# Optimization experiments

Hardware: AMD Instinct MI355X
Metric: run time of the kernel (lower is better)

Reference implementation:

```python
import jax, jax.numpy as jnp
import numpy as np

RADIUS = 0.4
NSAMPLE = 32


def setup_inputs() -> dict:
    key = jax.random.key(0)
    ks = jax.random.split(key, 6)
    B, N, C = 2, 16384, 64
    xyz = jax.random.normal(ks[0], (B, N, 3), jnp.float32)
    features = jax.random.normal(ks[1], (B, C, N), jnp.float32)

    def w(k, i, o):
        return jax.random.normal(k, (i, o), jnp.float32) * (1.0 / np.sqrt(i))

    W1 = w(ks[2], C + 3, 64)
    W2 = w(ks[3], 64, 64)
    W3 = w(ks[4], 64, 128)
    return {
        "xyz": xyz, "features": features,
        "W1": W1, "b1": jnp.zeros((64,), jnp.float32),
        "W2": W2, "b2": jnp.zeros((64,), jnp.float32),
        "W3": W3, "b3": jnp.zeros((128,), jnp.float32),
        "npoint": 4096,
    }


def ball_query(xyz, new_xyz, radius, nsample):
    """xyz [B,N,3], new_xyz [B,S,3] -> neighbor idx [B,S,nsample] int32.
    Replicates pointnet2 ball_query: first `nsample` points (in index order)
    within `radius` of each centroid; empty slots filled with the first hit
    (0 if no point is in range)."""
    N = xyz.shape[1]
    # squared distances [B,S,N] via ||a||^2 + ||b||^2 - 2 a.b
    d2 = (jnp.sum(new_xyz * new_xyz, -1)[:, :, None]
          + jnp.sum(xyz * xyz, -1)[:, None, :]
          - 2.0 * jnp.einsum('bsc,bnc->bsn', new_xyz, xyz))
    cand = jnp.where(d2 < radius * radius,
                     jnp.arange(N, dtype=jnp.int32), jnp.int32(N))
    neg_topk, _ = jax.lax.top_k(-cand, nsample)  # nsample smallest indices
    idx = -neg_topk
    first = idx[..., :1]
    idx = jnp.where(idx == N, first, idx)  # pad with first valid neighbor
    idx = jnp.where(idx == N, 0, idx)      # no neighbor at all -> 0
    return idx


def reference(xyz, features, W1, b1, W2, b2, W3, b3, npoint):
    B = xyz.shape[0]
    # sample_method=None, keep_first_half=False -> idx = arange(npoint)
    new_xyz = xyz[:, :npoint]                        # [B,S,3]
    idx = ball_query(jax.lax.stop_gradient(xyz),
                     jax.lax.stop_gradient(new_xyz), RADIUS, NSAMPLE)
    # group: gather neighbors, re-center xyz, concat features (use_xyz=True)
    grouped_xyz = jax.vmap(lambda p, i: p[i])(xyz, idx) - new_xyz[:, :, None]  # [B,S,K,3]
    feats_nc = features.transpose(0, 2, 1)           # [B,N,C]
    grouped_f = jax.vmap(lambda f, i: f[i])(feats_nc, idx)  # [B,S,K,C]
    g = jnp.concatenate([grouped_xyz, grouped_f], axis=-1)  # [B,S,K,3+C]
    # shared MLP (1x1 convs + ReLU)
    h = jax.nn.relu(jnp.einsum('bskc,cd->bskd', g, W1) + b1)
    h = jax.nn.relu(jnp.einsum('bskc,cd->bskd', h, W2) + b2)
    h = jax.nn.relu(jnp.einsum('bskc,cd->bskd', h, W3) + b3)
    new_features = jnp.max(h, axis=2).transpose(0, 2, 1)    # [B,128,S]
    samp_idx = jnp.tile(jnp.arange(npoint, dtype=jnp.int32), (B, 1))
    return new_xyz, new_features, samp_idx
```

## Files before the change

kernel.cpp:

```cpp
#include <hip/hip_runtime.h>

#define BB 2
#define NN 16384
#define CC 64
#define SS 4096
#define KK 32
#define R2 0.16f

#define GD   24
#define GC   (GD * GD * GD)
#define GCP  (GC + 4)
#define CAP  512
#define CAPL (CAP / 64)

typedef __bf16 bf16x8 __attribute__((ext_vector_type(8)));
typedef float  f32x4  __attribute__((ext_vector_type(4)));

#define MFMA(a, b, c) __builtin_amdgcn_mfma_f32_16x16x32_bf16((a), (b), (c), 0, 0, 0)

static __device__ __forceinline__ ushort f2bf(float f) {
    __bf16 h = (__bf16)f;
    return *(ushort*)&h;
}

static __device__ __forceinline__ int cellc(float x) {
    int i = (int)floorf(x * 2.5f + 12.0f);
    return i < 0 ? 0 : (i > GD - 1 ? GD - 1 : i);
}

#define WS_PTS4   0
#define WS_FEAT   524288
#define WS_W1T    4718592
#define WS_W2T    4730880
#define WS_W3T    4739072
#define WS_SPTS   4755456
#define WS_SSID   5279744
#define WS_CELLS  5410816
#define WS_OFF    5476352

#define T_PTS   (BB * NN)
#define T_W1    (T_PTS + 64 * 96)
#define T_W2    (T_W1 + 64 * 64)
#define T_W3    (T_W2 + 128 * 64)
#define T_NXYZ  (T_W3 + BB * SS * 3)
#define T_SIDX  (T_NXYZ + BB * SS)
#define T_ALL   (T_SIDX + BB * NN * 8)

__global__ __launch_bounds__(256) void prep_kernel(
        const float* __restrict__ xyz, const float* __restrict__ feat,
        const float* __restrict__ W1, const float* __restrict__ W2,
        const float* __restrict__ W3,
        float4* __restrict__ pts4, ushort* __restrict__ feat_nc,
        ushort* __restrict__ W1t, ushort* __restrict__ W2t,
        ushort* __restrict__ W3t,
        float* __restrict__ out_xyz, float* __restrict__ out_sidx,
        ushort* __restrict__ cells) {
    const int t = blockIdx.x * 256 + threadIdx.x;
    if (t < T_PTS) {
        const float* p = xyz + (size_t)t * 3;
        const float x = p[0], y = p[1], z = p[2];
        pts4[t] = make_float4(x, y, z, x * x + y * y + z * z);
        cells[t] = (ushort)((cellc(z) * GD + cellc(y)) * GD + cellc(x));
    } else if (t < T_W1) {
        const int i = t - T_PTS;
        const int n = i / 96, k = i - n * 96;
        float v = 0.0f;
        if (k < 64) v = W1[(3 + k) * 64 + n];
        else if (k < 67) v = W1[(k - 64) * 64 + n];
        W1t[n * 96 + k] = f2bf(v);
    } else if (t < T_W2) {
        const int i = t - T_W1;
        const int n = i >> 6, k = i & 63;
        W2t[n * 64 + k] = f2bf(W2[k * 64 + n]);
    } else if (t < T_W3) {
        const int i = t - T_W2;
        const int n = i >> 6, k = i & 63;
        W3t[n * 64 + k] = f2bf(W3[k * 128 + n]);
    } else if (t < T_NXYZ) {
        const int i = t - T_W3;
        const int b = i / (SS * 3), j = i - b * (SS * 3);
        out_xyz[i] = xyz[(size_t)b * NN * 3 + j];
    } else if (t < T_SIDX) {
        const int i = t - T_NXYZ;
        out_sidx[i] = (float)(i & (SS - 1));
    } else if (t < T_ALL) {
        const int j = t - T_SIDX;
        const int nl = j >> 3, c8 = j & 7;
        const int b = nl >> 14, n = nl & (NN - 1);
        const float* fb = feat + (size_t)b * CC * NN + n;
        uint u[4];
        #pragma unroll
        for (int q = 0; q < 4; ++q) {
            const float f0 = fb[(size_t)(c8 * 8 + 2 * q) * NN];
            const float f1 = fb[(size_t)(c8 * 8 + 2 * q + 1) * NN];
            u[q] = (uint)f2bf(f0) | ((uint)f2bf(f1) << 16);
        }
        *(uint4*)(feat_nc + (size_t)nl * 64 + c8 * 8) = make_uint4(u[0], u[1], u[2], u[3]);
    }
}

#define CH 14
__global__ __launch_bounds__(1024) void bin_kernel(
        const float4* __restrict__ pts4, const ushort* __restrict__ cells,
        float4* __restrict__ spts, int* __restrict__ ssid,
        uint* __restrict__ offs) {
    __shared__ uint hist[GC];
    __shared__ uint wsum[17];
    const int b = blockIdx.x, t = threadIdx.x;
    const ushort* cb = cells + (size_t)b * NN;

    for (int i = t; i < GC; i += 1024) hist[i] = 0u;
    __syncthreads();
    for (int i = t; i < NN; i += 1024) atomicAdd(&hist[cb[i]], 1u);
    __syncthreads();

    uint c[CH];
    uint s = 0;
    #pragma unroll
    for (int j = 0; j < CH; ++j) {
        const int ci = t * CH + j;
        c[j] = (ci < GC) ? hist[ci] : 0u;
        s += c[j];
    }
    const int lane = t & 63, wid = t >> 6;
    uint inc = s;
    #pragma unroll
    for (int o = 1; o < 64; o <<= 1) {
        const uint u = __shfl_up(inc, o);
        inc += (lane >= o) ? u : 0u;
    }
    if (lane == 63) wsum[wid] = inc;
    __syncthreads();
    if (t == 0) {
        uint r = 0;
        #pragma unroll
        for (int k = 0; k < 16; ++k) { const uint v2 = wsum[k]; wsum[k] = r; r += v2; }
    }
    __syncthreads();
    uint run = wsum[wid] + inc - s;
    uint* offb = offs + (size_t)b * GCP;
    #pragma unroll
    for (int j = 0; j < CH; ++j) {
        const int ci = t * CH + j;
        if (ci < GC) { offb[ci] = run; hist[ci] = run; run += c[j]; }
    }
    if (t == 1023) offb[GC] = NN;
    __syncthreads();

    for (int i = t; i < NN; i += 1024) {
        const int cell = cb[i];
        const uint pos = atomicAdd(&hist[cell], 1u);
        spts[(size_t)b * NN + pos] = pts4[(size_t)b * NN + i];
        ssid[(size_t)b * NN + pos] = i;
    }
}

__global__ __launch_bounds__(256, 2) void fused_kernel(
        const float4* __restrict__ pts4, const ushort* __restrict__ feat_nc,
        const float4* __restrict__ spts, const int* __restrict__ ssid,
        const uint* __restrict__ offs,
        const ushort* __restrict__ W1t, const ushort* __restrict__ W2t,
        const ushort* __restrict__ W3t,
        const float* __restrict__ b1, const float* __restrict__ b2,
        const float* __restrict__ b3, float* __restrict__ out_feat) {
    const int w = threadIdx.x >> 6, lane = threadIdx.x & 63;
    const int quad = lane >> 4, mrow = lane & 15;
    const int m = lane & 31, half = lane >> 5;

    __shared__ __align__(16) ushort ldsA[4][32 * 104];
    __shared__ float stage[128][5];
    ushort* gbuf = ldsA[w];
    int* hit = (int*)gbuf;

    const int xcd = blockIdx.x & 7;
    const int slot = blockIdx.x >> 3;
    const int b = xcd >> 2;
    const int s0 = ((xcd & 3) * 256 + slot) * 4;
    const int s = s0 + w;

    const float4* pb = pts4 + (size_t)b * NN;
    const ushort* fbase = feat_nc + (size_t)b * NN * 64;
    const unsigned long long ltmask = (1ull << lane) - 1ull;

    {
        const float4 c = pb[s];
        const int cx = cellc(c.x), cy = cellc(c.y), cz = cellc(c.z);
        const int x0 = cx - 1 < 0 ? 0 : cx - 1;
        const int x1 = cx + 1 > GD - 1 ? GD - 1 : cx + 1;
        const uint* off = offs + (size_t)b * GCP;
        const float4* sp = spts + (size_t)b * NN;
        const int* sidp = ssid + (size_t)b * NN;

        int rs[9], re[9], pre[10];
        pre[0] = 0;
        #pragma unroll
        for (int e = 0; e < 9; ++e) {
            const int z = cz + e / 3 - 1, y = cy + e % 3 - 1;
            const bool ok = (z >= 0) && (z < GD) && (y >= 0) && (y < GD);
            const int cbase = (z * GD + y) * GD;
            const int a = ok ? (int)off[cbase + x0] : 0;
            const int bnd = ok ? (int)off[cbase + x1 + 1] : 0;
            rs[e] = a;
            re[e] = ok ? bnd : a;
            pre[e + 1] = pre[e] + (re[e] - rs[e]);
        }
        const int tot = pre[9];

        int cnt = 0;
        for (int g0 = 0; g0 < tot; g0 += 64) {
            const int g = g0 + lane;
            int adj = rs[0];
            #pragma unroll
            for (int k = 1; k < 9; ++k) adj = (g >= pre[k]) ? (rs[k] - pre[k]) : adj;
            const bool act = g < tot;
            const int idx = act ? (g + adj) : 0;
            const float4 p = sp[idx];
            const int id = sidp[idx];
            const float d = c.w + p.w - 2.0f * (c.x * p.x + c.y * p.y + c.z * p.z);
            const bool h = act && (d < R2);
            const unsigned long long mk = __ballot(h);
            if (h) {
                const int pp = cnt + __popcll(mk & ltmask);
                if (pp < CAP) hit[pp] = id;
            }
            cnt += (int)__popcll(mk);
        }

        if (cnt > KK) {
            const int stored = cnt < CAP ? cnt : CAP;
            int v[CAPL];
            #pragma unroll
            for (int j = 0; j < CAPL; ++j) {
                const int q = j * 64 + lane;
                const int val = hit[q];
                v[j] = (q < stored) ? val : 0x7fffffff;
            }
            int lo = 0, hi = NN - 1;
            while (lo < hi) {
                const int mid = (lo + hi) >> 1;
                int cle = 0;
                #pragma unroll
                for (int j = 0; j < CAPL; ++j)
                    if (j * 64 < stored)
                        cle += (int)__popcll(__ballot(v[j] <= mid));
                if (cle >= KK) hi = mid; else lo = mid + 1;
            }
            int pos = 0;
            #pragma unroll
            for (int j = 0; j < CAPL; ++j) {
                if (j * 64 < stored) {
                    const bool sel = v[j] <= lo;
                    const unsigned long long mk = __ballot(sel);
                    if (sel) hit[pos + __popcll(mk & ltmask)] = v[j];
                    pos += (int)__popcll(mk);
                }
            }
        } else if (lane < KK) {
            const int vv = (cnt == 0) ? 0 : ((lane < cnt) ? hit[lane] : hit[0]);
            hit[lane] = vv;
        }
    }

    {
        const int sid = hit[m];
        const ushort* src = fbase + (size_t)sid * 64 + half * 32;
        ushort* dst = gbuf + m * 104 + half * 32;
        uint4 rows[4];
        #pragma unroll
        for (int i = 0; i < 4; ++i) rows[i] = *(const uint4*)(src + i * 8);
        const float4 p = pb[sid];
        const float4 cc = pb[s];
        #pragma unroll
        for (int i = 0; i < 4; ++i) *(uint4*)(dst + i * 8) = rows[i];
        if (half == 0) {
            bf16x8 rel = {(__bf16)(p.x - cc.x), (__bf16)(p.y - cc.y),
                          (__bf16)(p.z - cc.z), (__bf16)0.f,
                          (__bf16)0.f, (__bf16)0.f, (__bf16)0.f, (__bf16)0.f};
            *(bf16x8*)(gbuf + m * 104 + 64) = rel;
            *(uint4*)(gbuf + m * 104 + 88) = make_uint4(0, 0, 0, 0);
        } else {
            *(uint4*)(gbuf + m * 104 + 72) = make_uint4(0, 0, 0, 0);
            *(uint4*)(gbuf + m * 104 + 80) = make_uint4(0, 0, 0, 0);
        }
    }

    {
        f32x4 acc[2][4];
        #pragma unroll
        for (int nt = 0; nt < 4; ++nt) {
            const float bv = b1[nt * 16 + mrow];
            acc[0][nt] = (f32x4){bv, bv, bv, bv};
            acc[1][nt] = acc[0][nt];
        }
        #pragma unroll
        for (int ks = 0; ks < 3; ++ks) {
            const bf16x8 a0 = *(const bf16x8*)(gbuf + mrow * 104 + ks * 32 + quad * 8);
            const bf16x8 a1 = *(const bf16x8*)(gbuf + (16 + mrow) * 104 + ks * 32 + quad * 8);
            #pragma unroll
            for (int nt = 0; nt < 4; ++nt) {
                const bf16x8 wf = *(const bf16x8*)(W1t + (nt * 16 + mrow) * 96 + ks * 32 + quad * 8);
                acc[0][nt] = MFMA(a0, wf, acc[0][nt]);
                acc[1][nt] = MFMA(a1, wf, acc[1][nt]);
            }
        }
        #pragma unroll
        for (int mt = 0; mt < 2; ++mt)
            #pragma unroll
            for (int nt = 0; nt < 4; ++nt)
                #pragma unroll
                for (int r = 0; r < 4; ++r)
                    gbuf[(mt * 16 + quad * 4 + r) * 104 + nt * 16 + mrow] =
                        f2bf(fmaxf(acc[mt][nt][r], 0.0f));
    }

    {
        f32x4 acc[2][4];
        #pragma unroll
        for (int nt = 0; nt < 4; ++nt) {
            const float bv = b2[nt * 16 + mrow];
            acc[0][nt] = (f32x4){bv, bv, bv, bv};
            acc[1][nt] = acc[0][nt];
        }
        #pragma unroll
        for (int ks = 0; ks < 2; ++ks) {
            const bf16x8 a0 = *(const bf16x8*)(gbuf + mrow * 104 + ks * 32 + quad * 8);
            const bf16x8 a1 = *(const bf16x8*)(gbuf + (16 + mrow) * 104 + ks * 32 + quad * 8);
            #pragma unroll
            for (int nt = 0; nt < 4; ++nt) {
                const bf16x8 wf = *(const bf16x8*)(W2t + (nt * 16 + mrow) * 64 + ks * 32 + quad * 8);
                acc[0][nt] = MFMA(a0, wf, acc[0][nt]);
                acc[1][nt] = MFMA(a1, wf, acc[1][nt]);
            }
        }
        #pragma unroll
        for (int mt = 0; mt < 2; ++mt)
            #pragma unroll
            for (int nt = 0; nt < 4; ++nt)
                #pragma unroll
                for (int r = 0; r < 4; ++r)
                    gbuf[(mt * 16 + quad * 4 + r) * 104 + nt * 16 + mrow] =
                        f2bf(fmaxf(acc[mt][nt][r], 0.0f));
    }

    #pragma unroll
    for (int nh = 0; nh < 2; ++nh) {
        f32x4 acc[2][4];
        #pragma unroll
        for (int ntl = 0; ntl < 4; ++ntl) {
            const float bv = b3[(nh * 4 + ntl) * 16 + mrow];
            acc[0][ntl] = (f32x4){bv, bv, bv, bv};
            acc[1][ntl] = acc[0][ntl];
        }
        #pragma unroll
        for (int ks = 0; ks < 2; ++ks) {
            const bf16x8 a0 = *(const bf16x8*)(gbuf + mrow * 104 + ks * 32 + quad * 8);
            const bf16x8 a1 = *(const bf16x8*)(gbuf + (16 + mrow) * 104 + ks * 32 + quad * 8);
            #pragma unroll
            for (int ntl = 0; ntl < 4; ++ntl) {
                const bf16x8 wf = *(const bf16x8*)(
                    W3t + ((nh * 4 + ntl) * 16 + mrow) * 64 + ks * 32 + quad * 8);
                acc[0][ntl] = MFMA(a0, wf, acc[0][ntl]);
                acc[1][ntl] = MFMA(a1, wf, acc[1][ntl]);
            }
        }
        #pragma unroll
        for (int ntl = 0; ntl < 4; ++ntl) {
            const f32x4 v0 = acc[0][ntl], v1 = acc[1][ntl];
            float mx = fmaxf(fmaxf(v0[0], v0[1]), fmaxf(v0[2], v0[3]));
            mx = fmaxf(mx, fmaxf(fmaxf(v1[0], v1[1]), fmaxf(v1[2], v1[3])));
            mx = fmaxf(mx, __shfl_xor(mx, 16));
            mx = fmaxf(mx, __shfl_xor(mx, 32));
            mx = fmaxf(mx, 0.0f);
            if (quad == 0) stage[(nh * 4 + ntl) * 16 + mrow][w] = mx;
        }
    }
    __syncthreads();

    {
        const int ch = threadIdx.x & 127;
        const int hf = threadIdx.x >> 7;
        float* dst = out_feat + ((size_t)b * 128 + ch) * SS + s0 + hf * 2;
        *(float2*)dst = make_float2(stage[ch][hf * 2], stage[ch][hf * 2 + 1]);
    }
}

extern "C" void kernel_launch(void* const* d_in, const int* in_sizes, int n_in,
                              void* d_out, int out_size, void* d_ws, size_t ws_size,
                              hipStream_t stream) {
    const float* xyz  = (const float*)d_in[0];
    const float* feat = (const float*)d_in[1];
    const float* W1   = (const float*)d_in[2];
    const float* b1   = (const float*)d_in[3];
    const float* W2   = (const float*)d_in[4];
    const float* b2   = (const float*)d_in[5];
    const float* W3   = (const float*)d_in[6];
    const float* b3   = (const float*)d_in[7];

    float* out      = (float*)d_out;
    float* out_xyz  = out;
    float* out_feat = out + (size_t)BB * SS * 3;
    float* out_sidx = out_feat + (size_t)BB * 128 * SS;

    char* ws = (char*)d_ws;
    float4* pts4    = (float4*)(ws + WS_PTS4);
    ushort* feat_nc = (ushort*)(ws + WS_FEAT);
    ushort* W1t     = (ushort*)(ws + WS_W1T);
    ushort* W2t     = (ushort*)(ws + WS_W2T);
    ushort* W3t     = (ushort*)(ws + WS_W3T);
    float4* spts    = (float4*)(ws + WS_SPTS);
    int*    ssid    = (int*)(ws + WS_SSID);
    ushort* cells   = (ushort*)(ws + WS_CELLS);
    uint*   offs    = (uint*)(ws + WS_OFF);

    prep_kernel<<<(T_ALL + 255) / 256, 256, 0, stream>>>(
        xyz, feat, W1, W2, W3, pts4, feat_nc, W1t, W2t, W3t, out_xyz, out_sidx,
        cells);
    bin_kernel<<<BB, 1024, 0, stream>>>(pts4, cells, spts, ssid, offs);
    fused_kernel<<<BB * SS / 4, 256, 0, stream>>>(pts4, feat_nc, spts, ssid, offs,
                                                  W1t, W2t, W3t, b1, b2, b3,
                                                  out_feat);
}
```

Measured before the change: 172.2 us.

## Merge prep, binning and fused MLP into one cooperative persistent kernel

Replaces the three separate launches (prep, single-block-per-batch binning, fused query+MLP) with one cooperative kernel of 1024 blocks that uses grid syncs between phases. The histogram is packed as 16-bit counters in shared memory, and the scatter into sorted cells is spread across the whole grid using global atomics on a cursor array. The MLP phase loops over two tiles per block. The goal is to remove launch gaps and the serial two-block binning stage, at the cost of grid-wide barriers, global atomic contention, and a persistent grid capped at 4 blocks per CU.

```diff
diff --git a/kernel.cpp b/kernel.cpp
--- a/kernel.cpp
+++ b/kernel.cpp
@@ -1,4 +1,7 @@
 #include <hip/hip_runtime.h>
+#include <hip/hip_cooperative_groups.h>
+
+namespace cg = cooperative_groups;
 
 #define BB 2
 #define NN 16384
@@ -12,6 +15,9 @@
 #define GCP  (GC + 4)
 #define CAP  512
 #define CAPL (CAP / 64)
+
+#define GRID  1024
+#define TILES 2
 
 typedef __bf16 bf16x8 __attribute__((ext_vector_type(8)));
 typedef float  f32x4  __attribute__((ext_vector_type(4)));
@@ -37,6 +43,7 @@
 #define WS_SSID   5279744
 #define WS_CELLS  5410816
 #define WS_OFF    5476352
+#define WS_CURS   5586976
 
 #define T_PTS   (BB * NN)
 #define T_W1    (T_PTS + 64 * 96)
@@ -46,342 +53,357 @@
 #define T_SIDX  (T_NXYZ + BB * SS)
 #define T_ALL   (T_SIDX + BB * NN * 8)
 
-__global__ __launch_bounds__(256) void prep_kernel(
+#define CH 54
+
+__global__ __launch_bounds__(256, 4) void mega_kernel(
         const float* __restrict__ xyz, const float* __restrict__ feat,
-        const float* __restrict__ W1, const float* __restrict__ W2,
-        const float* __restrict__ W3,
-        float4* __restrict__ pts4, ushort* __restrict__ feat_nc,
-        ushort* __restrict__ W1t, ushort* __restrict__ W2t,
-        ushort* __restrict__ W3t,
-        float* __restrict__ out_xyz, float* __restrict__ out_sidx,
-        ushort* __restrict__ cells) {
-    const int t = blockIdx.x * 256 + threadIdx.x;
-    if (t < T_PTS) {
-        const float* p = xyz + (size_t)t * 3;
-        const float x = p[0], y = p[1], z = p[2];
-        pts4[t] = make_float4(x, y, z, x * x + y * y + z * z);
-        cells[t] = (ushort)((cellc(z) * GD + cellc(y)) * GD + cellc(x));
-    } else if (t < T_W1) {
-        const int i = t - T_PTS;
-        const int n = i / 96, k = i - n * 96;
-        float v = 0.0f;
-        if (k < 64) v = W1[(3 + k) * 64 + n];
-        else if (k < 67) v = W1[(k - 64) * 64 + n];
-        W1t[n * 96 + k] = f2bf(v);
-    } else if (t < T_W2) {
-        const int i = t - T_W1;
-        const int n = i >> 6, k = i & 63;
-        W2t[n * 64 + k] = f2bf(W2[k * 64 + n]);
-    } else if (t < T_W3) {
-        const int i = t - T_W2;
-        const int n = i >> 6, k = i & 63;
-        W3t[n * 64 + k] = f2bf(W3[k * 128 + n]);
-    } else if (t < T_NXYZ) {
-        const int i = t - T_W3;
-        const int b = i / (SS * 3), j = i - b * (SS * 3);
-        out_xyz[i] = xyz[(size_t)b * NN * 3 + j];
-    } else if (t < T_SIDX) {
-        const int i = t - T_NXYZ;
-        out_sidx[i] = (float)(i & (SS - 1));
-    } else if (t < T_ALL) {
-        const int j = t - T_SIDX;
-        const int nl = j >> 3, c8 = j & 7;
-        const int b = nl >> 14, n = nl & (NN - 1);
-        const float* fb = feat + (size_t)b * CC * NN + n;
-        uint u[4];
+        const float* __restrict__ W1, const float* __restrict__ b1,
+        const float* __restrict__ W2, const float* __restrict__ b2,
+        const float* __restrict__ W3, const float* __restrict__ b3,
+        char* __restrict__ ws, float* __restrict__ out) {
+    cg::grid_group gg = cg::this_grid();
+
+    float4* pts4    = (float4*)(ws + WS_PTS4);
+    ushort* feat_nc = (ushort*)(ws + WS_FEAT);
+    ushort* W1t     = (ushort*)(ws + WS_W1T);
+    ushort* W2t     = (ushort*)(ws + WS_W2T);
+    ushort* W3t     = (ushort*)(ws + WS_W3T);
+    float4* spts    = (float4*)(ws + WS_SPTS);
+    int*    ssid    = (int*)(ws + WS_SSID);
+    ushort* cells   = (ushort*)(ws + WS_CELLS);
+    uint*   offs    = (uint*)(ws + WS_OFF);
+    uint*   curs    = (uint*)(ws + WS_CURS);
+
+    float* out_xyz  = out;
+    float* out_feat = out + (size_t)BB * SS * 3;
+
+    __shared__ __align__(16) unsigned char smem[29184];
+
+    for (int t = blockIdx.x * 256 + threadIdx.x; t < T_ALL; t += GRID * 256) {
+        if (t < T_PTS) {
+            const float* p = xyz + (size_t)t * 3;
+            const float x = p[0], y = p[1], z = p[2];
+            pts4[t] = make_float4(x, y, z, x * x + y * y + z * z);
+            cells[t] = (ushort)((cellc(z) * GD + cellc(y)) * GD + cellc(x));
+        } else if (t < T_W1) {
+            const int i = t - T_PTS;
+            const int n = i / 96, k = i - n * 96;
+            float v = 0.0f;
+            if (k < 64) v = W1[(3 + k) * 64 + n];
+            else if (k < 67) v = W1[(k - 64) * 64 + n];
+            W1t[n * 96 + k] = f2bf(v);
+        } else if (t < T_W2) {
+            const int i = t - T_W1;
+            const int n = i >> 6, k = i & 63;
+            W2t[n * 64 + k] = f2bf(W2[k * 64 + n]);
+        } else if (t < T_W3) {
+            const int i = t - T_W2;
+            const int n = i >> 6, k = i & 63;
+            W3t[n * 64 + k] = f2bf(W3[k * 128 + n]);
+        } else if (t < T_NXYZ) {
+            const int i = t - T_W3;
+            const int b = i / (SS * 3), j = i - b * (SS * 3);
+            out_xyz[i] = xyz[(size_t)b * NN * 3 + j];
+        } else if (t < T_SIDX) {
+        } else {
+            const int j = t - T_SIDX;
+            const int nl = j >> 3, c8 = j & 7;
+            const int b = nl >> 14, n = nl & (NN - 1);
+            const float* fb = feat + (size_t)b * CC * NN + n;
+            uint u[4];
+            #pragma unroll
+            for (int q = 0; q < 4; ++q) {
+                const float f0 = fb[(size_t)(c8 * 8 + 2 * q) * NN];
+                const float f1 = fb[(size_t)(c8 * 8 + 2 * q + 1) * NN];
+                u[q] = (uint)f2bf(f0) | ((uint)f2bf(f1) << 16);
+            }
+            *(uint4*)(feat_nc + (size_t)nl * 64 + c8 * 8) =
+                make_uint4(u[0], u[1], u[2], u[3]);
+        }
+    }
+    gg.sync();
+
+    if (blockIdx.x < BB) {
+        uint* hist = (uint*)smem;
+        uint* wsum = (uint*)(smem + GC * 2);
+        const int b = blockIdx.x, t = threadIdx.x;
+        const int lane = t & 63, wid = t >> 6;
+        for (int i = t; i < GC / 2; i += 256) hist[i] = 0u;
+        __syncthreads();
+        const ushort* cb = cells + (size_t)b * NN;
+        for (int i = t; i < NN; i += 256) {
+            const uint c = cb[i];
+            atomicAdd(&hist[c >> 1], 1u << ((c & 1) << 4));
+        }
+        __syncthreads();
+        uint s = 0;
+        for (int j = 0; j < CH; ++j) {
+            const int ci = t * CH + j;
+            s += (hist[ci >> 1] >> ((ci & 1) << 4)) & 0xffffu;
+        }
+        uint inc = s;
         #pragma unroll
-        for (int q = 0; q < 4; ++q) {
-            const float f0 = fb[(size_t)(c8 * 8 + 2 * q) * NN];
-            const float f1 = fb[(size_t)(c8 * 8 + 2 * q + 1) * NN];
-            u[q] = (uint)f2bf(f0) | ((uint)f2bf(f1) << 16);
-        }
-        *(uint4*)(feat_nc + (size_t)nl * 64 + c8 * 8) = make_uint4(u[0], u[1], u[2], u[3]);
+        for (int o = 1; o < 64; o <<= 1) {
+            const uint u = __shfl_up(inc, o);
+            if (lane >= o) inc += u;
+        }
+        if (lane == 63) wsum[wid] = inc;
+        __syncthreads();
+        if (t == 0) {
+            uint r = 0;
+            #pragma unroll
+            for (int k = 0; k < 4; ++k) { const uint v = wsum[k]; wsum[k] = r; r += v; }
+        }
+        __syncthreads();
+        uint run = wsum[wid] + inc - s;
+        uint* offb = offs + (size_t)b * GCP;
+        uint* cub  = curs + (size_t)b * GC;
+        for (int j = 0; j < CH; ++j) {
+            const int ci = t * CH + j;
+            const uint cv = (hist[ci >> 1] >> ((ci & 1) << 4)) & 0xffffu;
+            offb[ci] = run; cub[ci] = run; run += cv;
+        }
+        if (t == 255) offb[GC] = NN;
     }
-}
-
-#define CH 14
-__global__ __launch_bounds__(1024) void bin_kernel(
-        const float4* __restrict__ pts4, const ushort* __restrict__ cells,
-        float4* __restrict__ spts, int* __restrict__ ssid,
-        uint* __restrict__ offs) {
-    __shared__ uint hist[GC];
-    __shared__ uint wsum[17];
-    const int b = blockIdx.x, t = threadIdx.x;
-    const ushort* cb = cells + (size_t)b * NN;
-
-    for (int i = t; i < GC; i += 1024) hist[i] = 0u;
-    __syncthreads();
-    for (int i = t; i < NN; i += 1024) atomicAdd(&hist[cb[i]], 1u);
-    __syncthreads();
-
-    uint c[CH];
-    uint s = 0;
-    #pragma unroll
-    for (int j = 0; j < CH; ++j) {
-        const int ci = t * CH + j;
-        c[j] = (ci < GC) ? hist[ci] : 0u;
-        s += c[j];
+    gg.sync();
+
+    for (int i = blockIdx.x * 256 + threadIdx.x; i < BB * NN; i += GRID * 256) {
+        const int b = i >> 14, n = i & (NN - 1);
+        const uint cell = cells[i];
+        const uint pos = atomicAdd(&curs[(size_t)b * GC + cell], 1u);
+        spts[(size_t)b * NN + pos] = pts4[i];
+        ssid[(size_t)b * NN + pos] = n;
     }
-    const int lane = t & 63, wid = t >> 6;
-    uint inc = s;
-    #pragma unroll
-    for (int o = 1; o < 64; o <<= 1) {
-        const uint u = __shfl_up(inc, o);
-        inc += (lane >= o) ? u : 0u;
-    }
-    if (lane == 63) wsum[wid] = inc;
-    __syncthreads();
-    if (t == 0) {
-        uint r = 0;
-        #pragma unroll
-        for (int k = 0; k < 16; ++k) { const uint v2 = wsum[k]; wsum[k] = r; r += v2; }
-    }
-    __syncthreads();
-    uint run = wsum[wid] + inc - s;
-    uint* offb = offs + (size_t)b * GCP;
-    #pragma unroll
-    for (int j = 0; j < CH; ++j) {
-        const int ci = t * CH + j;
-        if (ci < GC) { offb[ci] = run; hist[ci] = run; run += c[j]; }
-    }
-    if (t == 1023) offb[GC] = NN;
-    __syncthreads();
-
-    for (int i = t; i < NN; i += 1024) {
-        const int cell = cb[i];
-        const uint pos = atomicAdd(&hist[cell], 1u);
-        spts[(size_t)b * NN + pos] = pts4[(size_t)b * NN + i];
-        ssid[(size_t)b * NN + pos] = i;
-    }
-}
-
-__global__ __launch_bounds__(256, 2) void fused_kernel(
-        const float4* __restrict__ pts4, const ushort* __restrict__ feat_nc,
-        const float4* __restrict__ spts, const int* __restrict__ ssid,
-        const uint* __restrict__ offs,
-        const ushort* __restrict__ W1t, const ushort* __restrict__ W2t,
-        const ushort* __restrict__ W3t,
-        const float* __restrict__ b1, const float* __restrict__ b2,
-        const float* __restrict__ b3, float* __restrict__ out_feat) {
+    gg.sync();
+
+    ushort (*ldsA)[32 * 104] = (ushort(*)[32 * 104])smem;
+    float (*stage)[5] = (float(*)[5])(smem + 26624);
+
     const int w = threadIdx.x >> 6, lane = threadIdx.x & 63;
     const int quad = lane >> 4, mrow = lane & 15;
     const int m = lane & 31, half = lane >> 5;
-
-    __shared__ __align__(16) ushort ldsA[4][32 * 104];
-    __shared__ float stage[128][5];
     ushort* gbuf = ldsA[w];
     int* hit = (int*)gbuf;
-
-    const int xcd = blockIdx.x & 7;
-    const int slot = blockIdx.x >> 3;
-    const int b = xcd >> 2;
-    const int s0 = ((xcd & 3) * 256 + slot) * 4;
-    const int s = s0 + w;
-
-    const float4* pb = pts4 + (size_t)b * NN;
-    const ushort* fbase = feat_nc + (size_t)b * NN * 64;
     const unsigned long long ltmask = (1ull << lane) - 1ull;
 
-    {
-        const float4 c = pb[s];
-        const int cx = cellc(c.x), cy = cellc(c.y), cz = cellc(c.z);
-        const int x0 = cx - 1 < 0 ? 0 : cx - 1;
-        const int x1 = cx + 1 > GD - 1 ? GD - 1 : cx + 1;
-        const uint* off = offs + (size_t)b * GCP;
-        const float4* sp = spts + (size_t)b * NN;
-        const int* sidp = ssid + (size_t)b * NN;
-
-        int rs[9], re[9], pre[10];
-        pre[0] = 0;
+    for (int tt = 0; tt < TILES; ++tt) {
+        __syncthreads();
+        const int vt = tt * GRID + blockIdx.x;
+        const int xcd = vt & 7;
+        const int slot = vt >> 3;
+        const int b = xcd >> 2;
+        const int s0 = ((xcd & 3) * 256 + slot) * 4;
+        const int s = s0 + w;
+
+        const float4* pb = pts4 + (size_t)b * NN;
+        const ushort* fbase = feat_nc + (size_t)b * NN * 64;
+
+        {
+            const float4 c = pb[s];
+            const int cx = cellc(c.x), cy = cellc(c.y), cz = cellc(c.z);
+            const int x0 = cx - 1 < 0 ? 0 : cx - 1;
+            const int x1 = cx + 1 > GD - 1 ? GD - 1 : cx + 1;
+            const uint* off = offs + (size_t)b * GCP;
+            const float4* sp = spts + (size_t)b * NN;
+            const int* sidp = ssid + (size_t)b * NN;
+
+            int rs[9], re[9], pre[10];
+            pre[0] = 0;
+            #pragma unroll
+            for (int e = 0; e < 9; ++e) {
+                const int z = cz + e / 3 - 1, y = cy + e % 3 - 1;
+                const bool ok = (z >= 0) && (z < GD) && (y >= 0) && (y < GD);
+                const int cbase = (z * GD + y) * GD;
+                const int a = ok ? (int)off[cbase + x0] : 0;
+                const int bnd = ok ? (int)off[cbase + x1 + 1] : 0;
+                rs[e] = a;
+                re[e] = ok ? bnd : a;
+                pre[e + 1] = pre[e] + (re[e] - rs[e]);
+            }
+            const int tot = pre[9];
+
+            int cnt = 0;
+            for (int g0 = 0; g0 < tot; g0 += 64) {
+                const int g = g0 + lane;
+                int adj = rs[0];
+                #pragma unroll
+                for (int k = 1; k < 9; ++k) adj = (g >= pre[k]) ? (rs[k] - pre[k]) : adj;
+                const bool act = g < tot;
+                const int idx = act ? (g + adj) : 0;
+                const float4 p = sp[idx];
+                const int id = sidp[idx];
+                const float d = c.w + p.w - 2.0f * (c.x * p.x + c.y * p.y + c.z * p.z);
+                const bool h = act && (d < R2);
+                const unsigned long long mk = __ballot(h);
+                if (h) {
+                    const int pp = cnt + __popcll(mk & ltmask);
+                    if (pp < CAP) hit[pp] = id;
+                }
+                cnt += (int)__popcll(mk);
+            }
+
+            if (cnt > KK) {
+                const int stored = cnt < CAP ? cnt : CAP;
+                int v[CAPL];
+                #pragma unroll
+                for (int j = 0; j < CAPL; ++j) {
+                    const int q = j * 64 + lane;
+                    const int val = hit[q];
+                    v[j] = (q < stored) ? val : 0x7fffffff;
+                }
+                int lo = 0, hi = NN - 1;
+                while (lo < hi) {
+                    const int mid = (lo + hi) >> 1;
+                    int cle = 0;
+                    #pragma unroll
+                    for (int j = 0; j < CAPL; ++j)
+                        if (j * 64 < stored)
+                            cle += (int)__popcll(__ballot(v[j] <= mid));
+                    if (cle >= KK) hi = mid; else lo = mid + 1;
+                }
+                int pos = 0;
+                #pragma unroll
+                for (int j = 0; j < CAPL; ++j) {
+                    if (j * 64 < stored) {
+                        const bool sel = v[j] <= lo;
+                        const unsigned long long mk = __ballot(sel);
+                        if (sel) hit[pos + __popcll(mk & ltmask)] = v[j];
+                        pos += (int)__popcll(mk);
+                    }
+                }
+            } else if (lane < KK) {
+                const int vv = (cnt == 0) ? 0 : ((lane < cnt) ? hit[lane] : hit[0]);
+                hit[lane] = vv;
+            }
+        }
+
+        {
+            const int sid = hit[m];
+            const ushort* src = fbase + (size_t)sid * 64 + half * 32;
+            ushort* dst = gbuf + m * 104 + half * 32;
+            uint4 rows[4];
+            #pragma unroll
+            for (int i = 0; i < 4; ++i) rows[i] = *(const uint4*)(src + i * 8);
+            const float4 p = pb[sid];
+            const float4 cc = pb[s];
+            #pragma unroll
+            for (int i = 0; i < 4; ++i) *(uint4*)(dst + i * 8) = rows[i];
+            if (half == 0) {
+                bf16x8 rel = {(__bf16)(p.x - cc.x), (__bf16)(p.y - cc.y),
+                              (__bf16)(p.z - cc.z), (__bf16)0.f,
+                              (__bf16)0.f, (__bf16)0.f, (__bf16)0.f, (__bf16)0.f};
+                *(bf16x8*)(gbuf + m * 104 + 64) = rel;
+                *(uint4*)(gbuf + m * 104 + 88) = make_uint4(0, 0, 0, 0);
+            } else {
+                *(uint4*)(gbuf + m * 104 + 72) = make_uint4(0, 0, 0, 0);
+                *(uint4*)(gbuf + m * 104 + 80) = make_uint4(0, 0, 0, 0);
+            }
+        }
+
+        {
+            f32x4 acc[2][4];
+            #pragma unroll
+            for (int nt = 0; nt < 4; ++nt) {
+                const float bv = b1[nt * 16 + mrow];
+                acc[0][nt] = (f32x4){bv, bv, bv, bv};
+                acc[1][nt] = acc[0][nt];
+            }
+            #pragma unroll
+            for (int ks = 0; ks < 3; ++ks) {
+                const bf16x8 a0 = *(const bf16x8*)(gbuf + mrow * 104 + ks * 32 + quad * 8);
+                const bf16x8 a1 = *(const bf16x8*)(gbuf + (16 + mrow) * 104 + ks * 32 + quad * 8);
+                #pragma unroll
+                for (int nt = 0; nt < 4; ++nt) {
+                    const bf16x8 wf = *(const bf16x8*)(W1t + (nt * 16 + mrow) * 96 + ks * 32 + quad * 8);
+                    acc[0][nt] = MFMA(a0, wf, acc[0][nt]);
+                    acc[1][nt] = MFMA(a1, wf, acc[1][nt]);
+                }
+            }
+            #pragma unroll
+            for (int mt = 0; mt < 2; ++mt)
+                #pragma unroll
+                for (int nt = 0; nt < 4; ++nt)
+                    #pragma unroll
+                    for (int r = 0; r < 4; ++r)
+                        gbuf[(mt * 16 + quad * 4 + r) * 104 + nt * 16 + mrow] =
+                            f2bf(fmaxf(acc[mt][nt][r], 0.0f));
+        }
+
+        {
+            f32x4 acc[2][4];
+            #pragma unroll
+            for (int nt = 0; nt < 4; ++nt) {
+                const float bv = b2[nt * 16 + mrow];
+                acc[0][nt] = (f32x4){bv, bv, bv, bv};
+                acc[1][nt] = acc[0][nt];
+            }
+            #pragma unroll
+            for (int ks = 0; ks < 2; ++ks) {
+                const bf16x8 a0 = *(const bf16x8*)(gbuf + mrow * 104 + ks * 32 + quad * 8);
+                const bf16x8 a1 = *(const bf16x8*)(gbuf + (16 + mrow) * 104 + ks * 32 + quad * 8);
+                #pragma unroll
+                for (int nt = 0; nt < 4; ++nt) {
+                    const bf16x8 wf = *(const bf16x8*)(W2t + (nt * 16 + mrow) * 64 + ks * 32 + quad * 8);
+                    acc[0][nt] = MFMA(a0, wf, acc[0][nt]);
+                    acc[1][nt] = MFMA(a1, wf, acc[1][nt]);
+                }
+            }
+            #pragma unroll
+            for (int mt = 0; mt < 2; ++mt)
+                #pragma unroll
+                for (int nt = 0; nt < 4; ++nt)
+                    #pragma unroll
+                    for (int r = 0; r < 4; ++r)
+                        gbuf[(mt * 16 + quad * 4 + r) * 104 + nt * 16 + mrow] =
+                            f2bf(fmaxf(acc[mt][nt][r], 0.0f));
+        }
+
         #pragma unroll
-        for (int e = 0; e < 9; ++e) {
-            const int z = cz + e / 3 - 1, y = cy + e % 3 - 1;
-            const bool ok = (z >= 0) && (z < GD) && (y >= 0) && (y < GD);
-            const int cbase = (z * GD + y) * GD;
-            const int a = ok ? (int)off[cbase + x0] : 0;
-            const int bnd = ok ? (int)off[cbase + x1 + 1] : 0;
-            rs[e] = a;
-            re[e] = ok ? bnd : a;
-            pre[e + 1] = pre[e] + (re[e] - rs[e]);
-        }
-        const int tot = pre[9];
-
-        int cnt = 0;
-        for (int g0 = 0; g0 < tot; g0 += 64) {
-            const int g = g0 + lane;
-            int adj = rs[0];
-            #pragma unroll
-            for (int k = 1; k < 9; ++k) adj = (g >= pre[k]) ? (rs[k] - pre[k]) : adj;
-            const bool act = g < tot;
-            const int idx = act ? (g + adj) : 0;
-            const float4 p = sp[idx];
-            const int id = sidp[idx];
-            const float d = c.w + p.w - 2.0f * (c.x * p.x + c.y * p.y + c.z * p.z);
-            const bool h = act && (d < R2);
-            const unsigned long long mk = __ballot(h);
-            if (h) {
-                const int pp = cnt + __popcll(mk & ltmask);
-                if (pp < CAP) hit[pp] = id;
-            }
-            cnt += (int)__popcll(mk);
-        }
-
-        if (cnt > KK) {
-            const int stored = cnt < CAP ? cnt : CAP;
-            int v[CAPL];
-            #pragma unroll
-            for (int j = 0; j < CAPL; ++j) {
-                const int q = j * 64 + lane;
-                const int val = hit[q];
-                v[j] = (q < stored) ? val : 0x7fffffff;
-            }
-            int lo = 0, hi = NN - 1;
-            while (lo < hi) {
-                const int mid = (lo + hi) >> 1;
-                int cle = 0;
-                #pragma unroll
-                for (int j = 0; j < CAPL; ++j)
-                    if (j * 64 < stored)
-                        cle += (int)__popcll(__ballot(v[j] <= mid));
-                if (cle >= KK) hi = mid; else lo = mid + 1;
-            }
-            int pos = 0;
-            #pragma unroll
-            for (int j = 0; j < CAPL; ++j) {
-                if (j * 64 < stored) {
-                    const bool sel = v[j] <= lo;
-                    const unsigned long long mk = __ballot(sel);
-                    if (sel) hit[pos + __popcll(mk & ltmask)] = v[j];
-                    pos += (int)__popcll(mk);
-                }
-            }
-        } else if (lane < KK) {
-            const int vv = (cnt == 0) ? 0 : ((lane < cnt) ? hit[lane] : hit[0]);
-            hit[lane] = vv;
+        for (int nh = 0; nh < 2; ++nh) {
+            f32x4 acc[2][4];
+            #pragma unroll
+            for (int ntl = 0; ntl < 4; ++ntl) {
+                const float bv = b3[(nh * 4 + ntl) * 16 + mrow];
+                acc[0][ntl] = (f32x4){bv, bv, bv, bv};
+                acc[1][ntl] = acc[0][ntl];
+            }
+            #pragma unroll
+            for (int ks = 0; ks < 2; ++ks) {
+                const bf16x8 a0 = *(const bf16x8*)(gbuf + mrow * 104 + ks * 32 + quad * 8);
+                const bf16x8 a1 = *(const bf16x8*)(gbuf + (16 + mrow) * 104 + ks * 32 + quad * 8);
+                #pragma unroll
+                for (int ntl = 0; ntl < 4; ++ntl) {
+                    const bf16x8 wf = *(const bf16x8*)(
+                        W3t + ((nh * 4 + ntl) * 16 + mrow) * 64 + ks * 32 + quad * 8);
+                    acc[0][ntl] = MFMA(a0, wf, acc[0][ntl]);
+                    acc[1][ntl] = MFMA(a1, wf, acc[1][ntl]);
+                }
+            }
+            #pragma unroll
+            for (int ntl = 0; ntl < 4; ++ntl) {
+                const f32x4 v0 = acc[0][ntl], v1 = acc[1][ntl];
+                float mx = fmaxf(fmaxf(v0[0], v0[1]), fmaxf(v0[2], v0[3]));
+                mx = fmaxf(mx, fmaxf(fmaxf(v1[0], v1[1]), fmaxf(v1[2], v1[3])));
+                mx = fmaxf(mx, __shfl_xor(mx, 16));
+                mx = fmaxf(mx, __shfl_xor(mx, 32));
+                mx = fmaxf(mx, 0.0f);
+                if (quad == 0) stage[(nh * 4 + ntl) * 16 + mrow][w] = mx;
+            }
+        }
+        __syncthreads();
+
+        {
+            const int ch = threadIdx.x & 127;
+            const int hf = threadIdx.x >> 7;
+            float* dst = out_feat + ((size_t)b * 128 + ch) * SS + s0 + hf * 2;
+            *(float2*)dst = make_float2(stage[ch][hf * 2], stage[ch][hf * 2 + 1]);
         }
     }
-
-    {
-        const int sid = hit[m];
-        const ushort* src = fbase + (size_t)sid * 64 + half * 32;
-        ushort* dst = gbuf + m * 104 + half * 32;
-        uint4 rows[4];
-        #pragma unroll
-        for (int i = 0; i < 4; ++i) rows[i] = *(const uint4*)(src + i * 8);
-        const float4 p = pb[sid];
-        const float4 cc = pb[s];
-        #pragma unroll
-        for (int i = 0; i < 4; ++i) *(uint4*)(dst + i * 8) = rows[i];
-        if (half == 0) {
-            bf16x8 rel = {(__bf16)(p.x - cc.x), (__bf16)(p.y - cc.y),
-                          (__bf16)(p.z - cc.z), (__bf16)0.f,
-                          (__bf16)0.f, (__bf16)0.f, (__bf16)0.f, (__bf16)0.f};
-            *(bf16x8*)(gbuf + m * 104 + 64) = rel;
-            *(uint4*)(gbuf + m * 104 + 88) = make_uint4(0, 0, 0, 0);
-        } else {
-            *(uint4*)(gbuf + m * 104 + 72) = make_uint4(0, 0, 0, 0);
-            *(uint4*)(gbuf + m * 104 + 80) = make_uint4(0, 0, 0, 0);
-        }
-    }
-
-    {
-        f32x4 acc[2][4];
-        #pragma unroll
-        for (int nt = 0; nt < 4; ++nt) {
-            const float bv = b1[nt * 16 + mrow];
-            acc[0][nt] = (f32x4){bv, bv, bv, bv};
-            acc[1][nt] = acc[0][nt];
-        }
-        #pragma unroll
-        for (int ks = 0; ks < 3; ++ks) {
-            const bf16x8 a0 = *(const bf16x8*)(gbuf + mrow * 104 + ks * 32 + quad * 8);
-            const bf16x8 a1 = *(const bf16x8*)(gbuf + (16 + mrow) * 104 + ks * 32 + quad * 8);
-            #pragma unroll
-            for (int nt = 0; nt < 4; ++nt) {
-                const bf16x8 wf = *(const bf16x8*)(W1t + (nt * 16 + mrow) * 96 + ks * 32 + quad * 8);
-                acc[0][nt] = MFMA(a0, wf, acc[0][nt]);
-                acc[1][nt] = MFMA(a1, wf, acc[1][nt]);
-            }
-        }
-        #pragma unroll
-        for (int mt = 0; mt < 2; ++mt)
-            #pragma unroll
-            for (int nt = 0; nt < 4; ++nt)
-                #pragma unroll
-                for (int r = 0; r < 4; ++r)
-                    gbuf[(mt * 16 + quad * 4 + r) * 104 + nt * 16 + mrow] =
-                        f2bf(fmaxf(acc[mt][nt][r], 0.0f));
-    }
-
-    {
-        f32x4 acc[2][4];
-        #pragma unroll
-        for (int nt = 0; nt < 4; ++nt) {
-            const float bv = b2[nt * 16 + mrow];
-            acc[0][nt] = (f32x4){bv, bv, bv, bv};
-            acc[1][nt] = acc[0][nt];
-        }
-        #pragma unroll
-        for (int ks = 0; ks < 2; ++ks) {
-            const bf16x8 a0 = *(const bf16x8*)(gbuf + mrow * 104 + ks * 32 + quad * 8);
-            const bf16x8 a1 = *(const bf16x8*)(gbuf + (16 + mrow) * 104 + ks * 32 + quad * 8);
-            #pragma unroll
-            for (int nt = 0; nt < 4; ++nt) {
-                const bf16x8 wf = *(const bf16x8*)(W2t + (nt * 16 + mrow) * 64 + ks * 32 + quad * 8);
-                acc[0][nt] = MFMA(a0, wf, acc[0][nt]);
-                acc[1][nt] = MFMA(a1, wf, acc[1][nt]);
-            }
-        }
-        #pragma unroll
-        for (int mt = 0; mt < 2; ++mt)
-            #pragma unroll
-            for (int nt = 0; nt < 4; ++nt)
-                #pragma unroll
-                for (int r = 0; r < 4; ++r)
-                    gbuf[(mt * 16 + quad * 4 + r) * 104 + nt * 16 + mrow] =
-                        f2bf(fmaxf(acc[mt][nt][r], 0.0f));
-    }
-
-    #pragma unroll
-    for (int nh = 0; nh < 2; ++nh) {
-        f32x4 acc[2][4];
-        #pragma unroll
-        for (int ntl = 0; ntl < 4; ++ntl) {
-            const float bv = b3[(nh * 4 + ntl) * 16 + mrow];
-            acc[0][ntl] = (f32x4){bv, bv, bv, bv};
-            acc[1][ntl] = acc[0][ntl];
-        }
-        #pragma unroll
-        for (int ks = 0; ks < 2; ++ks) {
-            const bf16x8 a0 = *(const bf16x8*)(gbuf + mrow * 104 + ks * 32 + quad * 8);
-            const bf16x8 a1 = *(const bf16x8*)(gbuf + (16 + mrow) * 104 + ks * 32 + quad * 8);
-            #pragma unroll
-            for (int ntl = 0; ntl < 4; ++ntl) {
-                const bf16x8 wf = *(const bf16x8*)(
-                    W3t + ((nh * 4 + ntl) * 16 + mrow) * 64 + ks * 32 + quad * 8);
-                acc[0][ntl] = MFMA(a0, wf, acc[0][ntl]);
-                acc[1][ntl] = MFMA(a1, wf, acc[1][ntl]);
-            }
-        }
-        #pragma unroll
-        for (int ntl = 0; ntl < 4; ++ntl) {
-            const f32x4 v0 = acc[0][ntl], v1 = acc[1][ntl];
-            float mx = fmaxf(fmaxf(v0[0], v0[1]), fmaxf(v0[2], v0[3]));
-            mx = fmaxf(mx, fmaxf(fmaxf(v1[0], v1[1]), fmaxf(v1[2], v1[3])));
-            mx = fmaxf(mx, __shfl_xor(mx, 16));
-            mx = fmaxf(mx, __shfl_xor(mx, 32));
-            mx = fmaxf(mx, 0.0f);
-            if (quad == 0) stage[(nh * 4 + ntl) * 16 + mrow][w] = mx;
-        }
-    }
-    __syncthreads();
-
-    {
-        const int ch = threadIdx.x & 127;
-        const int hf = threadIdx.x >> 7;
-        float* dst = out_feat + ((size_t)b * 128 + ch) * SS + s0 + hf * 2;
-        *(float2*)dst = make_float2(stage[ch][hf * 2], stage[ch][hf * 2 + 1]);
-    }
+}
+
+__global__ __launch_bounds__(256) void sidx_kernel(float* __restrict__ out_sidx) {
+    const int i = blockIdx.x * 256 + threadIdx.x;
+    out_sidx[i] = (float)(i & (SS - 1));
 }
 
 extern "C" void kernel_launch(void* const* d_in, const int* in_sizes, int n_in,
@@ -396,27 +418,16 @@
     const float* W3   = (const float*)d_in[6];
     const float* b3   = (const float*)d_in[7];
 
-    float* out      = (float*)d_out;
-    float* out_xyz  = out;
-    float* out_feat = out + (size_t)BB * SS * 3;
-    float* out_sidx = out_feat + (size_t)BB * 128 * SS;
-
-    char* ws = (char*)d_ws;
-    float4* pts4    = (float4*)(ws + WS_PTS4);
-    ushort* feat_nc = (ushort*)(ws + WS_FEAT);
-    ushort* W1t     = (ushort*)(ws + WS_W1T);
-    ushort* W2t     = (ushort*)(ws + WS_W2T);
-    ushort* W3t     = (ushort*)(ws + WS_W3T);
-    float4* spts    = (float4*)(ws + WS_SPTS);
-    int*    ssid    = (int*)(ws + WS_SSID);
-    ushort* cells   = (ushort*)(ws + WS_CELLS);
-    uint*   offs    = (uint*)(ws + WS_OFF);
-
-    prep_kernel<<<(T_ALL + 255) / 256, 256, 0, stream>>>(
-        xyz, feat, W1, W2, W3, pts4, feat_nc, W1t, W2t, W3t, out_xyz, out_sidx,
-        cells);
-    bin_kernel<<<BB, 1024, 0, stream>>>(pts4, cells, spts, ssid, offs);
-    fused_kernel<<<BB * SS / 4, 256, 0, stream>>>(pts4, feat_nc, spts, ssid, offs,
-                                                  W1t, W2t, W3t, b1, b2, b3,
-                                                  out_feat);
+    char*  ws  = (char*)d_ws;
+    float* out = (float*)d_out;
+    float* out_sidx = out + (size_t)BB * SS * 3 + (size_t)BB * 128 * SS;
+
+    void* args[] = {
+        (void*)&xyz, (void*)&feat,
+        (void*)&W1, (void*)&b1, (void*)&W2, (void*)&b2, (void*)&W3, (void*)&b3,
+        (void*)&ws, (void*)&out
+    };
+    hipLaunchCooperativeKernel(reinterpret_cast<void*>(mega_kernel),
+                               dim3(GRID), dim3(256), args, 0, stream);
+    sidx_kernel<<<BB * SS / 256, 256, 0, stream>>>(out_sidx);
 }
```

Result: slower. 527.7 us (+206.5%).

## Replace counting-sort bin kernel with fixed-capacity per-cell neighbor lists

Applied to the files above, without the earlier changes.

Drops the two-block counting-sort bin kernel. Points are now appended to fixed-capacity per-cell index lists with global atomics inside the prep kernel, after a memset of the cell counters. The ball query walks the 27 neighbouring cells' lists and gathers point coordinates through the stored index. This removes a poorly parallel launch and its prefix scan. In exchange it adds a dependent indirect load and more range-select work per query. Any cell holding more than 112 points silently drops the extra points.

```diff
diff --git a/kernel.cpp b/kernel.cpp
--- a/kernel.cpp
+++ b/kernel.cpp
@@ -9,7 +9,7 @@
 
 #define GD   24
 #define GC   (GD * GD * GD)
-#define GCP  (GC + 4)
+#define CAPC 112
 #define CAP  512
 #define CAPL (CAP / 64)
 
@@ -33,10 +33,8 @@
 #define WS_W1T    4718592
 #define WS_W2T    4730880
 #define WS_W3T    4739072
-#define WS_SPTS   4755456
-#define WS_SSID   5279744
-#define WS_CELLS  5410816
-#define WS_OFF    5476352
+#define WS_CNT    4755456
+#define WS_LIST   4866048
 
 #define T_PTS   (BB * NN)
 #define T_W1    (T_PTS + 64 * 96)
@@ -54,13 +52,17 @@
         ushort* __restrict__ W1t, ushort* __restrict__ W2t,
         ushort* __restrict__ W3t,
         float* __restrict__ out_xyz, float* __restrict__ out_sidx,
-        ushort* __restrict__ cells) {
+        uint* __restrict__ counts, int* __restrict__ list) {
     const int t = blockIdx.x * 256 + threadIdx.x;
     if (t < T_PTS) {
         const float* p = xyz + (size_t)t * 3;
         const float x = p[0], y = p[1], z = p[2];
         pts4[t] = make_float4(x, y, z, x * x + y * y + z * z);
-        cells[t] = (ushort)((cellc(z) * GD + cellc(y)) * GD + cellc(x));
+        const int cell = (cellc(z) * GD + cellc(y)) * GD + cellc(x);
+        const int b = t >> 14, n = t & (NN - 1);
+        const uint rank = atomicAdd(&counts[(size_t)b * GC + cell], 1u);
+        if (rank < CAPC)
+            list[((size_t)b * GC + cell) * CAPC + rank] = n;
     } else if (t < T_W1) {
         const int i = t - T_PTS;
         const int n = i / 96, k = i - n * 96;
@@ -99,66 +101,9 @@
     }
 }
 
-#define CH 14
-__global__ __launch_bounds__(1024) void bin_kernel(
-        const float4* __restrict__ pts4, const ushort* __restrict__ cells,
-        float4* __restrict__ spts, int* __restrict__ ssid,
-        uint* __restrict__ offs) {
-    __shared__ uint hist[GC];
-    __shared__ uint wsum[17];
-    const int b = blockIdx.x, t = threadIdx.x;
-    const ushort* cb = cells + (size_t)b * NN;
-
-    for (int i = t; i < GC; i += 1024) hist[i] = 0u;
-    __syncthreads();
-    for (int i = t; i < NN; i += 1024) atomicAdd(&hist[cb[i]], 1u);
-    __syncthreads();
-
-    uint c[CH];
-    uint s = 0;
-    #pragma unroll
-    for (int j = 0; j < CH; ++j) {
-        const int ci = t * CH + j;
-        c[j] = (ci < GC) ? hist[ci] : 0u;
-        s += c[j];
-    }
-    const int lane = t & 63, wid = t >> 6;
-    uint inc = s;
-    #pragma unroll
-    for (int o = 1; o < 64; o <<= 1) {
-        const uint u = __shfl_up(inc, o);
-        inc += (lane >= o) ? u : 0u;
-    }
-    if (lane == 63) wsum[wid] = inc;
-    __syncthreads();
-    if (t == 0) {
-        uint r = 0;
-        #pragma unroll
-        for (int k = 0; k < 16; ++k) { const uint v2 = wsum[k]; wsum[k] = r; r += v2; }
-    }
-    __syncthreads();
-    uint run = wsum[wid] + inc - s;
-    uint* offb = offs + (size_t)b * GCP;
-    #pragma unroll
-    for (int j = 0; j < CH; ++j) {
-        const int ci = t * CH + j;
-        if (ci < GC) { offb[ci] = run; hist[ci] = run; run += c[j]; }
-    }
-    if (t == 1023) offb[GC] = NN;
-    __syncthreads();
-
-    for (int i = t; i < NN; i += 1024) {
-        const int cell = cb[i];
-        const uint pos = atomicAdd(&hist[cell], 1u);
-        spts[(size_t)b * NN + pos] = pts4[(size_t)b * NN + i];
-        ssid[(size_t)b * NN + pos] = i;
-    }
-}
-
 __global__ __launch_bounds__(256, 2) void fused_kernel(
         const float4* __restrict__ pts4, const ushort* __restrict__ feat_nc,
-        const float4* __restrict__ spts, const int* __restrict__ ssid,
-        const uint* __restrict__ offs,
+        const uint* __restrict__ counts, const int* __restrict__ list,
         const ushort* __restrict__ W1t, const ushort* __restrict__ W2t,
         const ushort* __restrict__ W3t,
         const float* __restrict__ b1, const float* __restrict__ b2,
@@ -185,37 +130,34 @@
     {
         const float4 c = pb[s];
         const int cx = cellc(c.x), cy = cellc(c.y), cz = cellc(c.z);
-        const int x0 = cx - 1 < 0 ? 0 : cx - 1;
-        const int x1 = cx + 1 > GD - 1 ? GD - 1 : cx + 1;
-        const uint* off = offs + (size_t)b * GCP;
-        const float4* sp = spts + (size_t)b * NN;
-        const int* sidp = ssid + (size_t)b * NN;
-
-        int rs[9], re[9], pre[10];
+        const uint* cntb = counts + (size_t)b * GC;
+        const int* listb = list + (size_t)b * GC * CAPC;
+
+        int pre[28], A[27];
         pre[0] = 0;
         #pragma unroll
-        for (int e = 0; e < 9; ++e) {
-            const int z = cz + e / 3 - 1, y = cy + e % 3 - 1;
-            const bool ok = (z >= 0) && (z < GD) && (y >= 0) && (y < GD);
-            const int cbase = (z * GD + y) * GD;
-            const int a = ok ? (int)off[cbase + x0] : 0;
-            const int bnd = ok ? (int)off[cbase + x1 + 1] : 0;
-            rs[e] = a;
-            re[e] = ok ? bnd : a;
-            pre[e + 1] = pre[e] + (re[e] - rs[e]);
-        }
-        const int tot = pre[9];
+        for (int e = 0; e < 27; ++e) {
+            const int z = cz + e / 9 - 1;
+            const int y = cy + (e / 3) % 3 - 1;
+            const int x = cx + e % 3 - 1;
+            const bool ok = ((unsigned)z < GD) && ((unsigned)y < GD) && ((unsigned)x < GD);
+            const int ci = (z * GD + y) * GD + x;
+            int cn = ok ? (int)cntb[ci] : 0;
+            cn = cn < CAPC ? cn : CAPC;
+            A[e] = ci * CAPC - pre[e];
+            pre[e + 1] = pre[e] + cn;
+        }
+        const int tot = pre[27];
 
         int cnt = 0;
         for (int g0 = 0; g0 < tot; g0 += 64) {
             const int g = g0 + lane;
-            int adj = rs[0];
-            #pragma unroll
-            for (int k = 1; k < 9; ++k) adj = (g >= pre[k]) ? (rs[k] - pre[k]) : adj;
+            int adj = A[0];
+            #pragma unroll
+            for (int k = 1; k < 27; ++k) adj = (g >= pre[k]) ? A[k] : adj;
             const bool act = g < tot;
-            const int idx = act ? (g + adj) : 0;
-            const float4 p = sp[idx];
-            const int id = sidp[idx];
+            const int id = act ? listb[g + adj] : 0;
+            const float4 p = pb[id];
             const float d = c.w + p.w - 2.0f * (c.x * p.x + c.y * p.y + c.z * p.z);
             const bool h = act && (d < R2);
             const unsigned long long mk = __ballot(h);
@@ -407,16 +349,14 @@
     ushort* W1t     = (ushort*)(ws + WS_W1T);
     ushort* W2t     = (ushort*)(ws + WS_W2T);
     ushort* W3t     = (ushort*)(ws + WS_W3T);
-    float4* spts    = (float4*)(ws + WS_SPTS);
-    int*    ssid    = (int*)(ws + WS_SSID);
-    ushort* cells   = (ushort*)(ws + WS_CELLS);
-    uint*   offs    = (uint*)(ws + WS_OFF);
-
+    uint*   counts  = (uint*)(ws + WS_CNT);
+    int*    list    = (int*)(ws + WS_LIST);
+
+    hipMemsetAsync(counts, 0, (size_t)BB * GC * 4, stream);
     prep_kernel<<<(T_ALL + 255) / 256, 256, 0, stream>>>(
         xyz, feat, W1, W2, W3, pts4, feat_nc, W1t, W2t, W3t, out_xyz, out_sidx,
-        cells);
-    bin_kernel<<<BB, 1024, 0, stream>>>(pts4, cells, spts, ssid, offs);
-    fused_kernel<<<BB * SS / 4, 256, 0, stream>>>(pts4, feat_nc, spts, ssid, offs,
+        counts, list);
+    fused_kernel<<<BB * SS / 4, 256, 0, stream>>>(pts4, feat_nc, counts, list,
                                                   W1t, W2t, W3t, b1, b2, b3,
                                                   out_feat);
 }
```

Result: faster. 148.5 us (-13.8%).
